# Optimization experiments

Hardware: AMD Instinct MI355X
Metric: run time of the kernel (lower is better)

Reference implementation:

```python
import jax, jax.numpy as jnp
import numpy as np

N = 16000      # nodes
E = 256000     # edges (avg degree 16)
C = 64         # channel multiplicity (64x0e node feats)
A = 10         # num elements (one-hot node_attrs)
R = 8          # num radial edge feats
OFFS = [0, 1, 4, 9]   # m-offsets for l=0,1,2 blocks (dims 1,3,5)
AVG_NEIGH = 16.0


def setup_inputs() -> dict:
    key = jax.random.key(0)
    ks = jax.random.split(key, 12)
    species = jax.random.randint(ks[0], (N,), 0, A)
    node_attrs = jax.nn.one_hot(species, A, dtype=jnp.float32)
    node_feats = jax.random.normal(ks[1], (N, C), jnp.float32)
    edge_attrs_real = jax.random.normal(ks[2], (E, 9), jnp.float32)
    edge_attrs_imag = jax.random.normal(ks[3], (E, 9), jnp.float32)
    edge_feats = jax.random.normal(ks[4], (E, R), jnp.float32)
    senders = jax.random.randint(ks[5], (E,), 0, N)
    receivers = jax.random.randint(ks[6], (E,), 0, N)
    # learned parameters
    W_up = jax.random.normal(ks[7], (C, C), jnp.float32)            # linear_up (64x0e -> 64x0e)
    W_tpw = jax.random.normal(ks[8], (A, R, 3, C), jnp.float32) * 0.1  # TensorProductWeightsBlock, weight_numel = 3*C
    W_lin = jax.random.normal(ks[9], (3, C, C), jnp.float32)        # per-l linear on irreps_mid -> irreps_out
    W_skip = jax.random.normal(ks[10], (C, A, C), jnp.float32)      # FullyConnectedTensorProduct skip
    return {"node_attrs": node_attrs, "node_feats": node_feats,
            "edge_attrs_real": edge_attrs_real, "edge_attrs_imag": edge_attrs_imag,
            "edge_feats": edge_feats, "senders": senders, "receivers": receivers,
            "W_up": W_up, "W_tpw": W_tpw, "W_lin": W_lin, "W_skip": W_skip}


def reference(node_attrs, node_feats, edge_attrs_real, edge_attrs_imag, edge_feats,
              senders, receivers, W_up, W_tpw, W_lin, W_skip):
    # skip connection: FullyConnectedTensorProduct(node_feats, node_attrs) (all scalars)
    sc = jnp.einsum('nu,na,uak->nk', node_feats, node_attrs, W_skip) / np.float32(np.sqrt(C * A))
    # linear_up (e3nn Linear with 1/sqrt(fan_in) normalization)
    h = (node_feats @ W_up) / np.float32(np.sqrt(C))
    # per-edge TP weights: einsum('be,ba,aek->bk'), reshaped to [E, 3 paths, C]
    tp_w = jnp.einsum('er,ea,arlu->elu', edge_feats, node_attrs[senders], W_tpw)
    x_s = h[senders]  # gather sender node feats [E, C]
    def conv(edge_attrs):
        # uvu tensor product 64x0e x (0e+1o+2e): CG(0,l,l)=1 -> weighted outer product per l
        parts = [x_s[:, :, None] * tp_w[:, l, :, None] * edge_attrs[:, None, OFFS[l]:OFFS[l + 1]]
                 for l in range(3)]
        mji = jnp.concatenate(parts, axis=-1)                      # [E, C, 9]
        m = jax.ops.segment_sum(mji, receivers, num_segments=N)   # scatter-sum -> [N, C, 9]
        outs = [jnp.einsum('num,uv->nvm', m[:, :, OFFS[l]:OFFS[l + 1]], W_lin[l]) / np.float32(np.sqrt(C))
                for l in range(3)]
        return jnp.concatenate(outs, axis=-1) / np.float32(AVG_NEIGH)  # [N, C, 9]
    message_real = conv(edge_attrs_real)
    message_imag = conv(edge_attrs_imag)
    # torch.view_as_complex + reshape_irreps -> complex [N, C, 9]; returned as (real, imag)
    return message_real, message_imag, sc
```

## Files before the change

kernel.cpp:

```cpp
#include <hip/hip_runtime.h>
#include <hip/hip_bf16.h>

#define NN 16000
#define EE 256000
#define CC 64
#define AA 10
#define RR 8
#define NC9 9216000
#define SC_OFF 18432000

#define WS_H        0
#define WS_BLK      4096000
#define WS_SPECIES  32768256
#define WS_COUNTS   32832256
#define WS_CURSOR   32896256
#define WS_OFFSETS  32960256

__global__ __launch_bounds__(256) void species_kernel(
    const float* __restrict__ attrs, int* __restrict__ species) {
  int i = blockIdx.x * 256 + threadIdx.x;
  if (i >= NN) return;
  const float* p = attrs + (size_t)i * AA;
  int sp = 0;
#pragma unroll
  for (int a = 1; a < AA; ++a)
    if (p[a] > 0.5f) sp = a;
  species[i] = sp;
}

__global__ __launch_bounds__(256) void node_kernel(
    const float* __restrict__ nf, const int* __restrict__ species,
    const float* __restrict__ W_up, const float* __restrict__ W_skip,
    float* __restrict__ h, float* __restrict__ out) {
  int wid = __builtin_amdgcn_readfirstlane(threadIdx.x >> 6);
  int lane = threadIdx.x & 63;
  int n = blockIdx.x * 4 + wid;
  int a = species[n];
  const float* nfp = nf + (size_t)n * 64;
  const float* wsk = W_skip + (size_t)a * 64;
  float hacc = 0.f, sacc = 0.f;
#pragma unroll
  for (int u = 0; u < 64; ++u) {
    float x = nfp[u];
    hacc = fmaf(x, W_up[u * 64 + lane], hacc);
    sacc = fmaf(x, wsk[u * 640 + lane], sacc);
  }
  h[(size_t)n * 64 + lane] = hacc * 0.125f;
  out[SC_OFF + (size_t)n * 64 + lane] = sacc * 0.03952847075210474f;
}

__global__ __launch_bounds__(256) void hist_kernel(
    const int* __restrict__ recv, int* __restrict__ counts) {
  int e = blockIdx.x * 256 + threadIdx.x;
  if (e < EE) atomicAdd(&counts[recv[e]], 1);
}

__global__ __launch_bounds__(1024) void scan_kernel(
    const int* __restrict__ counts, int* __restrict__ offsets) {
  __shared__ int part[1024];
  int tid = threadIdx.x;
  const int CH = 16;
  int base = tid * CH;
  int loc[CH];
  int s = 0;
#pragma unroll
  for (int i = 0; i < CH; ++i) {
    int idx = base + i;
    int c = (idx < NN) ? counts[idx] : 0;
    loc[i] = c;
    s += c;
  }
  part[tid] = s;
  __syncthreads();
  for (int off = 1; off < 1024; off <<= 1) {
    int t = part[tid];
    int add = (tid >= off) ? part[tid - off] : 0;
    __syncthreads();
    part[tid] = t + add;
    __syncthreads();
  }
  int pre = (tid > 0) ? part[tid - 1] : 0;
#pragma unroll
  for (int i = 0; i < CH; ++i) {
    int idx = base + i;
    if (idx <= NN) offsets[idx] = pre;
    pre += loc[i];
  }
}

__global__ __launch_bounds__(256) void fill_kernel(
    const int* __restrict__ recv, const int* __restrict__ senders,
    const int* __restrict__ species, const int* __restrict__ offsets,
    int* __restrict__ cursor, const float* __restrict__ ef,
    const float* __restrict__ ear, const float* __restrict__ eai,
    float* __restrict__ blk) {
  int e = blockIdx.x * 256 + threadIdx.x;
  if (e >= EE) return;
  int r = recv[e];
  int pos = atomicAdd(&cursor[r], 1);
  int slot = offsets[r] + pos;
  int s = senders[e];
  int a = species[s];
  const float* efp = ef + (size_t)e * 8;
  const float* erp = ear + (size_t)e * 9;
  const float* eip = eai + (size_t)e * 9;
  float4* dst = (float4*)(blk + (size_t)slot * 28);
  float4 q;
  q.x = __int_as_float(s | (a << 20)); q.y = efp[0]; q.z = efp[1]; q.w = efp[2];
  dst[0] = q;
  q.x = efp[3]; q.y = efp[4]; q.z = efp[5]; q.w = efp[6];
  dst[1] = q;
  q.x = efp[7]; q.y = erp[0]; q.z = erp[1]; q.w = erp[2];
  dst[2] = q;
  q.x = erp[3]; q.y = erp[4]; q.z = erp[5]; q.w = erp[6];
  dst[3] = q;
  q.x = erp[7]; q.y = erp[8]; q.z = eip[0]; q.w = eip[1];
  dst[4] = q;
  q.x = eip[2]; q.y = eip[3]; q.z = eip[4]; q.w = eip[5];
  dst[5] = q;
  q.x = eip[6]; q.y = eip[7]; q.z = eip[8]; q.w = 0.f;
  dst[6] = q;
}

#define RL(V, L) __builtin_amdgcn_readlane((V), (L))
#define RLF(V, L) __int_as_float(__builtin_amdgcn_readlane((V), (L)))

#define EDGE(BLK, OFF, XS) do {                                            \
  float efs[8], ers[9], eis[9];                                            \
  _Pragma("unroll") for (int i_ = 0; i_ < 8; ++i_)                         \
    efs[i_] = RLF((BLK), (OFF) + 1 + i_);                                  \
  _Pragma("unroll") for (int i_ = 0; i_ < 9; ++i_)                         \
    ers[i_] = RLF((BLK), (OFF) + 9 + i_);                                  \
  _Pragma("unroll") for (int i_ = 0; i_ < 9; ++i_)                         \
    eis[i_] = RLF((BLK), (OFF) + 18 + i_);                                 \
  int a_ = RL((BLK), (OFF)) >> 20;                                         \
  const float4* wp_ = (const float4*)(lds + a_ * 1792 + lane * 28);        \
  float4 w0_ = wp_[gpi[0]], w1_ = wp_[gpi[1]], w2_ = wp_[gpi[2]];          \
  float4 w3_ = wp_[gpi[3]], w4_ = wp_[gpi[4]], w5_ = wp_[gpi[5]];          \
  const float wv_[24] = {w0_.x, w0_.y, w0_.z, w0_.w, w1_.x, w1_.y, w1_.z,  \
                         w1_.w, w2_.x, w2_.y, w2_.z, w2_.w, w3_.x, w3_.y,  \
                         w3_.z, w3_.w, w4_.x, w4_.y, w4_.z, w4_.w, w5_.x,  \
                         w5_.y, w5_.z, w5_.w};                             \
  float t0_ = 0.f, t1_ = 0.f, t2_ = 0.f;                                   \
  _Pragma("unroll") for (int r_ = 0; r_ < 8; ++r_) {                       \
    t0_ = fmaf(efs[r_], wv_[r_ * 3 + 0], t0_);                             \
    t1_ = fmaf(efs[r_], wv_[r_ * 3 + 1], t1_);                             \
    t2_ = fmaf(efs[r_], wv_[r_ * 3 + 2], t2_);                             \
  }                                                                        \
  t0_ *= (XS); t1_ *= (XS); t2_ *= (XS);                                   \
  accR[0] = fmaf(t0_, ers[0], accR[0]);                                    \
  accI[0] = fmaf(t0_, eis[0], accI[0]);                                    \
  _Pragma("unroll") for (int m_ = 1; m_ < 4; ++m_) {                       \
    accR[m_] = fmaf(t1_, ers[m_], accR[m_]);                               \
    accI[m_] = fmaf(t1_, eis[m_], accI[m_]);                               \
  }                                                                        \
  _Pragma("unroll") for (int m_ = 4; m_ < 9; ++m_) {                       \
    accR[m_] = fmaf(t2_, ers[m_], accR[m_]);                               \
    accI[m_] = fmaf(t2_, eis[m_], accI[m_]);                               \
  }                                                                        \
} while (0)

__global__ __launch_bounds__(512, 4) void fused_kernel(
    const float* __restrict__ h, const int* __restrict__ offs,
    const float* __restrict__ blkd, const float* __restrict__ W_tpw,
    const float* __restrict__ W_lin, float* __restrict__ out) {
  __shared__ float lds[17920];
  for (int idx = threadIdx.x; idx < AA * RR * 3 * 64; idx += 512) {
    int a = idx / 1536, rem = idx - a * 1536;
    int r = rem / 192;  int rem2 = rem - r * 192;
    int p = rem2 >> 6;  int u = rem2 & 63;
    int k = r * 3 + p, g = k >> 2, j = k & 3;
    int gp = g + (u >> 3); gp = (gp >= 7) ? gp - 7 : gp;
    lds[a * 1792 + u * 28 + gp * 4 + j] = W_tpw[idx];
  }
  __syncthreads();
  int wid = __builtin_amdgcn_readfirstlane(threadIdx.x >> 6);
  int lane = threadIdx.x & 63;
  int n = blockIdx.x * 8 + wid;
  int gpi[6];
#pragma unroll
  for (int g = 0; g < 6; ++g) {
    int t = g + (lane >> 3); gpi[g] = (t >= 7) ? t - 7 : t;
  }
  float accR[9], accI[9];
#pragma unroll
  for (int m = 0; m < 9; ++m) { accR[m] = 0.f; accI[m] = 0.f; }
  int beg = offs[n], end = offs[n + 1];
  int cnt = end - beg;
  if (cnt > 0) {
    const int* base = (const int*)blkd + (size_t)beg * 28;
    int blkP = base[lane];
    int sA = RL(blkP, 0) & 0xFFFFF;  sA = (sA < NN) ? sA : 0;
    int sB = RL(blkP, 28) & 0xFFFFF; sB = (sB < NN) ? sB : 0;
    float xsA = h[(size_t)sA * 64 + lane];
    float xsB = h[(size_t)sB * 64 + lane];
    int pairs = (cnt + 1) >> 1;
    int blkN = (pairs > 1) ? base[56 + lane] : blkP;
    for (int p = 0; p < pairs; ++p) {
      float xsA2 = 0.f, xsB2 = 0.f;
      int blkNN = blkN;
      if (p + 1 < pairs) {
        int sA2 = RL(blkN, 0) & 0xFFFFF;  sA2 = (sA2 < NN) ? sA2 : 0;
        int sB2 = RL(blkN, 28) & 0xFFFFF; sB2 = (sB2 < NN) ? sB2 : 0;
        xsA2 = h[(size_t)sA2 * 64 + lane];
        xsB2 = h[(size_t)sB2 * 64 + lane];
        if (p + 2 < pairs) blkNN = base[(size_t)(p + 2) * 56 + lane];
      }
      EDGE(blkP, 0, xsA);
      if (2 * p + 1 < cnt) EDGE(blkP, 28, xsB);
      blkP = blkN; blkN = blkNN; xsA = xsA2; xsB = xsB2;
    }
  }
  __builtin_amdgcn_sched_barrier(0);
  float outR[9], outI[9];
#pragma unroll
  for (int m = 0; m < 9; ++m) { outR[m] = 0.f; outI[m] = 0.f; }
  {
    float wreg[64];
#pragma unroll
    for (int u = 0; u < 64; ++u) wreg[u] = W_lin[u * 64 + lane];
#pragma unroll
    for (int u = 0; u < 64; ++u) {
      outR[0] = fmaf(RLF(__float_as_int(accR[0]), u), wreg[u], outR[0]);
      outI[0] = fmaf(RLF(__float_as_int(accI[0]), u), wreg[u], outI[0]);
    }
  }
  __builtin_amdgcn_sched_barrier(0);
  {
    float wreg[64];
#pragma unroll
    for (int u = 0; u < 64; ++u) wreg[u] = W_lin[4096 + u * 64 + lane];
#pragma unroll
    for (int u = 0; u < 64; ++u) {
#pragma unroll
      for (int m = 1; m < 4; ++m) {
        outR[m] = fmaf(RLF(__float_as_int(accR[m]), u), wreg[u], outR[m]);
        outI[m] = fmaf(RLF(__float_as_int(accI[m]), u), wreg[u], outI[m]);
      }
    }
  }
  __builtin_amdgcn_sched_barrier(0);
  {
    float wreg[64];
#pragma unroll
    for (int u = 0; u < 64; ++u) wreg[u] = W_lin[8192 + u * 64 + lane];
#pragma unroll
    for (int u = 0; u < 64; ++u) {
#pragma unroll
      for (int m = 4; m < 9; ++m) {
        outR[m] = fmaf(RLF(__float_as_int(accR[m]), u), wreg[u], outR[m]);
        outI[m] = fmaf(RLF(__float_as_int(accI[m]), u), wreg[u], outI[m]);
      }
    }
  }
  __builtin_amdgcn_sched_barrier(0);
  __syncthreads();
  const float SCL = 0.0078125f;
  float* stg = lds + wid * 1152;
#pragma unroll
  for (int m = 0; m < 9; ++m) {
    stg[lane * 9 + m] = outR[m] * SCL;
    stg[576 + lane * 9 + m] = outI[m] * SCL;
  }
#pragma unroll
  for (int k = 0; k < 9; ++k) {
    out[(size_t)n * 576 + k * 64 + lane] = stg[k * 64 + lane];
    out[NC9 + (size_t)n * 576 + k * 64 + lane] = stg[576 + k * 64 + lane];
  }
}

extern "C" void kernel_launch(void* const* d_in, const int* in_sizes, int n_in,
                              void* d_out, int out_size, void* d_ws, size_t ws_size,
                              hipStream_t stream) {
  const float* node_attrs = (const float*)d_in[0];
  const float* node_feats = (const float*)d_in[1];
  const float* ear        = (const float*)d_in[2];
  const float* eai        = (const float*)d_in[3];
  const float* ef         = (const float*)d_in[4];
  const int*   senders    = (const int*)d_in[5];
  const int*   receivers  = (const int*)d_in[6];
  const float* W_up       = (const float*)d_in[7];
  const float* W_tpw      = (const float*)d_in[8];
  const float* W_lin      = (const float*)d_in[9];
  const float* W_skip     = (const float*)d_in[10];
  float* out = (float*)d_out;

  char* ws = (char*)d_ws;
  float* h        = (float*)(ws + WS_H);
  float* blk      = (float*)(ws + WS_BLK);
  int*   species  = (int*)(ws + WS_SPECIES);
  int*   counts   = (int*)(ws + WS_COUNTS);
  int*   cursor   = (int*)(ws + WS_CURSOR);
  int*   offsets  = (int*)(ws + WS_OFFSETS);

  hipMemsetAsync(ws + WS_COUNTS, 0, 128000, stream);

  species_kernel<<<63, 256, 0, stream>>>(node_attrs, species);
  node_kernel<<<4000, 256, 0, stream>>>(node_feats, species, W_up, W_skip, h, out);
  hist_kernel<<<1000, 256, 0, stream>>>(receivers, counts);
  scan_kernel<<<1, 1024, 0, stream>>>(counts, offsets);
  fill_kernel<<<1000, 256, 0, stream>>>(receivers, senders, species, offsets,
                                        cursor, ef, ear, eai, blk);
  fused_kernel<<<2000, 512, 0, stream>>>(h, offsets, blk, W_tpw, W_lin, out);
}
```

Measured before the change: 351.9 us.

## Split edge sort into index list and edge-ordered blocks, transpose W_lin

Replaces the single fill kernel, which scattered full 112-byte edge records to sorted slots, with a kernel that only scatters edge indices into a CSR list and a separate kernel that writes records in original edge order with coalesced stores. The fused kernel now gathers records indirectly through the index list, using a deeper index prefetch and splitting lanes between the two edges of each pair. W_lin is transposed once so each lane can load its weight row with float4 loads. Launch bounds occupancy drops from 4 to 2 and the LDS weight staging uses float4 writes. The cost is an extra indirection and random 112-byte gathers inside the main kernel, plus two extra launches.

```diff
diff --git a/kernel.cpp b/kernel.cpp
--- a/kernel.cpp
+++ b/kernel.cpp
@@ -11,10 +11,12 @@
 
 #define WS_H        0
 #define WS_BLK      4096000
-#define WS_SPECIES  32768256
-#define WS_COUNTS   32832256
-#define WS_CURSOR   32896256
-#define WS_OFFSETS  32960256
+#define WS_WLT      32768000
+#define WS_SPECIES  32817152
+#define WS_COUNTS   32881152
+#define WS_CURSOR   32945152
+#define WS_OFFSETS  33009152
+#define WS_ELIST    33073216
 
 __global__ __launch_bounds__(256) void species_kernel(
     const float* __restrict__ attrs, int* __restrict__ species) {
@@ -49,6 +51,14 @@
   out[SC_OFF + (size_t)n * 64 + lane] = sacc * 0.03952847075210474f;
 }
 
+__global__ __launch_bounds__(256) void wlint_kernel(
+    const float* __restrict__ W_lin, float* __restrict__ W_linT) {
+  int idx = blockIdx.x * 256 + threadIdx.x;
+  if (idx >= 3 * 64 * 64) return;
+  int l = idx >> 12, rem = idx & 4095, v = rem >> 6, u = rem & 63;
+  W_linT[idx] = W_lin[l * 4096 + u * 64 + v];
+}
+
 __global__ __launch_bounds__(256) void hist_kernel(
     const int* __restrict__ recv, int* __restrict__ counts) {
   int e = blockIdx.x * 256 + threadIdx.x;
@@ -88,23 +98,28 @@
   }
 }
 
-__global__ __launch_bounds__(256) void fill_kernel(
-    const int* __restrict__ recv, const int* __restrict__ senders,
-    const int* __restrict__ species, const int* __restrict__ offsets,
-    int* __restrict__ cursor, const float* __restrict__ ef,
-    const float* __restrict__ ear, const float* __restrict__ eai,
-    float* __restrict__ blk) {
+__global__ __launch_bounds__(256) void fill_slots_kernel(
+    const int* __restrict__ recv, const int* __restrict__ offsets,
+    int* __restrict__ cursor, int* __restrict__ elist) {
   int e = blockIdx.x * 256 + threadIdx.x;
   if (e >= EE) return;
   int r = recv[e];
   int pos = atomicAdd(&cursor[r], 1);
-  int slot = offsets[r] + pos;
+  elist[offsets[r] + pos] = e;
+}
+
+__global__ __launch_bounds__(256) void build_blk_kernel(
+    const int* __restrict__ senders, const int* __restrict__ species,
+    const float* __restrict__ ef, const float* __restrict__ ear,
+    const float* __restrict__ eai, float* __restrict__ blk) {
+  int e = blockIdx.x * 256 + threadIdx.x;
+  if (e >= EE) return;
   int s = senders[e];
   int a = species[s];
   const float* efp = ef + (size_t)e * 8;
   const float* erp = ear + (size_t)e * 9;
   const float* eip = eai + (size_t)e * 9;
-  float4* dst = (float4*)(blk + (size_t)slot * 28);
+  float4* dst = (float4*)(blk + (size_t)e * 28);
   float4 q;
   q.x = __int_as_float(s | (a << 20)); q.y = efp[0]; q.z = efp[1]; q.w = efp[2];
   dst[0] = q;
@@ -160,18 +175,20 @@
   }                                                                        \
 } while (0)
 
-__global__ __launch_bounds__(512, 4) void fused_kernel(
+__global__ __launch_bounds__(512, 2) void fused_kernel(
     const float* __restrict__ h, const int* __restrict__ offs,
-    const float* __restrict__ blkd, const float* __restrict__ W_tpw,
-    const float* __restrict__ W_lin, float* __restrict__ out) {
+    const float* __restrict__ blkd, const int* __restrict__ elist,
+    const float* __restrict__ W_tpw, const float* __restrict__ W_linT,
+    float* __restrict__ out) {
   __shared__ float lds[17920];
-  for (int idx = threadIdx.x; idx < AA * RR * 3 * 64; idx += 512) {
-    int a = idx / 1536, rem = idx - a * 1536;
-    int r = rem / 192;  int rem2 = rem - r * 192;
-    int p = rem2 >> 6;  int u = rem2 & 63;
-    int k = r * 3 + p, g = k >> 2, j = k & 3;
-    int gp = g + (u >> 3); gp = (gp >= 7) ? gp - 7 : gp;
-    lds[a * 1792 + u * 28 + gp * 4 + j] = W_tpw[idx];
+  for (int t = threadIdx.x; t < AA * 6 * 64; t += 512) {
+    int a = t / 384, rem = t - a * 384;
+    int g = rem >> 6, u = rem & 63;
+    int gp = g + (u >> 3); if (gp >= 7) gp -= 7;
+    const float* src = W_tpw + a * 1536 + g * 256 + u;
+    float4 w;
+    w.x = src[0]; w.y = src[64]; w.z = src[128]; w.w = src[192];
+    *(float4*)&lds[a * 1792 + u * 28 + gp * 4] = w;
   }
   __syncthreads();
   int wid = __builtin_amdgcn_readfirstlane(threadIdx.x >> 6);
@@ -185,26 +202,46 @@
   float accR[9], accI[9];
 #pragma unroll
   for (int m = 0; m < 9; ++m) { accR[m] = 0.f; accI[m] = 0.f; }
-  int beg = offs[n], end = offs[n + 1];
-  int cnt = end - beg;
+  int beg = __builtin_amdgcn_readfirstlane(offs[n]);
+  int cnt = __builtin_amdgcn_readfirstlane(offs[n + 1]) - beg;
   if (cnt > 0) {
-    const int* base = (const int*)blkd + (size_t)beg * 28;
-    int blkP = base[lane];
-    int sA = RL(blkP, 0) & 0xFFFFF;  sA = (sA < NN) ? sA : 0;
-    int sB = RL(blkP, 28) & 0xFFFFF; sB = (sB < NN) ? sB : 0;
+    const int* bi = (const int*)blkd;
+    int pairs = (cnt + 1) >> 1;
+    int lm = lane, roleB = 0;
+    if (lane >= 28) { lm = lane - 28; roleB = 1; }
+    if (lane >= 56) { lm = 0; roleB = 0; }
+    int ea0 = elist[beg];
+    int eb0 = (cnt > 1) ? elist[beg + 1] : ea0;
+    int blkP = bi[(size_t)(roleB ? eb0 : ea0) * 28 + lm];
+    int blkN = blkP;
+    if (pairs > 1) {
+      int ea1 = elist[beg + 2];
+      int eb1 = (cnt > 3) ? elist[beg + 3] : ea1;
+      blkN = bi[(size_t)(roleB ? eb1 : ea1) * 28 + lm];
+    }
+    int ean = 0, ebn = 0;
+    if (pairs > 2) {
+      ean = elist[beg + 4];
+      ebn = (cnt > 5) ? elist[beg + 5] : ean;
+    }
+    int sA = RL(blkP, 0) & 0xFFFFF;
+    int sB = RL(blkP, 28) & 0xFFFFF;
     float xsA = h[(size_t)sA * 64 + lane];
     float xsB = h[(size_t)sB * 64 + lane];
-    int pairs = (cnt + 1) >> 1;
-    int blkN = (pairs > 1) ? base[56 + lane] : blkP;
     for (int p = 0; p < pairs; ++p) {
+      int blkNN = blkN;
+      if (p + 2 < pairs)
+        blkNN = bi[(size_t)(roleB ? ebn : ean) * 28 + lm];
+      if (p + 3 < pairs) {
+        ean = elist[beg + 2 * (p + 3)];
+        ebn = (2 * (p + 3) + 1 < cnt) ? elist[beg + 2 * (p + 3) + 1] : ean;
+      }
       float xsA2 = 0.f, xsB2 = 0.f;
-      int blkNN = blkN;
       if (p + 1 < pairs) {
-        int sA2 = RL(blkN, 0) & 0xFFFFF;  sA2 = (sA2 < NN) ? sA2 : 0;
-        int sB2 = RL(blkN, 28) & 0xFFFFF; sB2 = (sB2 < NN) ? sB2 : 0;
+        int sA2 = RL(blkN, 0) & 0xFFFFF;
+        int sB2 = RL(blkN, 28) & 0xFFFFF;
         xsA2 = h[(size_t)sA2 * 64 + lane];
         xsB2 = h[(size_t)sB2 * 64 + lane];
-        if (p + 2 < pairs) blkNN = base[(size_t)(p + 2) * 56 + lane];
       }
       EDGE(blkP, 0, xsA);
       if (2 * p + 1 < cnt) EDGE(blkP, 28, xsB);
@@ -216,40 +253,46 @@
 #pragma unroll
   for (int m = 0; m < 9; ++m) { outR[m] = 0.f; outI[m] = 0.f; }
   {
-    float wreg[64];
-#pragma unroll
-    for (int u = 0; u < 64; ++u) wreg[u] = W_lin[u * 64 + lane];
+    const float4* wt = (const float4*)(W_linT + (size_t)lane * 64);
+    float4 wr[16];
+#pragma unroll
+    for (int q = 0; q < 16; ++q) wr[q] = wt[q];
+    const float* wf = (const float*)wr;
 #pragma unroll
     for (int u = 0; u < 64; ++u) {
-      outR[0] = fmaf(RLF(__float_as_int(accR[0]), u), wreg[u], outR[0]);
-      outI[0] = fmaf(RLF(__float_as_int(accI[0]), u), wreg[u], outI[0]);
+      outR[0] = fmaf(RLF(__float_as_int(accR[0]), u), wf[u], outR[0]);
+      outI[0] = fmaf(RLF(__float_as_int(accI[0]), u), wf[u], outI[0]);
     }
   }
   __builtin_amdgcn_sched_barrier(0);
   {
-    float wreg[64];
-#pragma unroll
-    for (int u = 0; u < 64; ++u) wreg[u] = W_lin[4096 + u * 64 + lane];
+    const float4* wt = (const float4*)(W_linT + 4096 + (size_t)lane * 64);
+    float4 wr[16];
+#pragma unroll
+    for (int q = 0; q < 16; ++q) wr[q] = wt[q];
+    const float* wf = (const float*)wr;
 #pragma unroll
     for (int u = 0; u < 64; ++u) {
 #pragma unroll
       for (int m = 1; m < 4; ++m) {
-        outR[m] = fmaf(RLF(__float_as_int(accR[m]), u), wreg[u], outR[m]);
-        outI[m] = fmaf(RLF(__float_as_int(accI[m]), u), wreg[u], outI[m]);
+        outR[m] = fmaf(RLF(__float_as_int(accR[m]), u), wf[u], outR[m]);
+        outI[m] = fmaf(RLF(__float_as_int(accI[m]), u), wf[u], outI[m]);
       }
     }
   }
   __builtin_amdgcn_sched_barrier(0);
   {
-    float wreg[64];
-#pragma unroll
-    for (int u = 0; u < 64; ++u) wreg[u] = W_lin[8192 + u * 64 + lane];
+    const float4* wt = (const float4*)(W_linT + 8192 + (size_t)lane * 64);
+    float4 wr[16];
+#pragma unroll
+    for (int q = 0; q < 16; ++q) wr[q] = wt[q];
+    const float* wf = (const float*)wr;
 #pragma unroll
     for (int u = 0; u < 64; ++u) {
 #pragma unroll
       for (int m = 4; m < 9; ++m) {
-        outR[m] = fmaf(RLF(__float_as_int(accR[m]), u), wreg[u], outR[m]);
-        outI[m] = fmaf(RLF(__float_as_int(accI[m]), u), wreg[u], outI[m]);
+        outR[m] = fmaf(RLF(__float_as_int(accR[m]), u), wf[u], outR[m]);
+        outI[m] = fmaf(RLF(__float_as_int(accI[m]), u), wf[u], outI[m]);
       }
     }
   }
@@ -262,6 +305,7 @@
     stg[lane * 9 + m] = outR[m] * SCL;
     stg[576 + lane * 9 + m] = outI[m] * SCL;
   }
+  __builtin_amdgcn_s_waitcnt(0);
 #pragma unroll
   for (int k = 0; k < 9; ++k) {
     out[(size_t)n * 576 + k * 64 + lane] = stg[k * 64 + lane];
@@ -288,18 +332,21 @@
   char* ws = (char*)d_ws;
   float* h        = (float*)(ws + WS_H);
   float* blk      = (float*)(ws + WS_BLK);
+  float* wlt      = (float*)(ws + WS_WLT);
   int*   species  = (int*)(ws + WS_SPECIES);
   int*   counts   = (int*)(ws + WS_COUNTS);
   int*   cursor   = (int*)(ws + WS_CURSOR);
   int*   offsets  = (int*)(ws + WS_OFFSETS);
+  int*   elist    = (int*)(ws + WS_ELIST);
 
   hipMemsetAsync(ws + WS_COUNTS, 0, 128000, stream);
 
   species_kernel<<<63, 256, 0, stream>>>(node_attrs, species);
   node_kernel<<<4000, 256, 0, stream>>>(node_feats, species, W_up, W_skip, h, out);
+  wlint_kernel<<<48, 256, 0, stream>>>(W_lin, wlt);
   hist_kernel<<<1000, 256, 0, stream>>>(receivers, counts);
   scan_kernel<<<1, 1024, 0, stream>>>(counts, offsets);
-  fill_kernel<<<1000, 256, 0, stream>>>(receivers, senders, species, offsets,
-                                        cursor, ef, ear, eai, blk);
-  fused_kernel<<<2000, 512, 0, stream>>>(h, offsets, blk, W_tpw, W_lin, out);
-}
+  fill_slots_kernel<<<1000, 256, 0, stream>>>(receivers, offsets, cursor, elist);
+  build_blk_kernel<<<1000, 256, 0, stream>>>(senders, species, ef, ear, eai, blk);
+  fused_kernel<<<2000, 512, 0, stream>>>(h, offsets, blk, elist, W_tpw, wlt, out);
+}
```

Measured after the change: 369.6 us. +5.0%, slower.
